# Kernel tuning notes

Hardware: AMD Instinct MI355X
Metric: run time of the kernel (lower is better)

Reference implementation:

```python
import jax, jax.numpy as jnp
from jax import lax
import numpy as np

H = 32  # hidden size
D = 1   # input size


def setup_inputs() -> dict:
    key = jax.random.key(0)
    ks = jax.random.split(key, 7)
    B, T = 4096, 1024
    s_ih = 1.0 / np.sqrt(H)
    return {
        "x": jax.random.normal(ks[0], (B, T, D), dtype=jnp.float32),
        # PyTorch LSTM params, gate order i,f,g,o stacked along dim 0
        "W_ih": jax.random.uniform(ks[1], (4 * H, D), jnp.float32, -s_ih, s_ih),
        "W_hh": jax.random.uniform(ks[2], (4 * H, H), jnp.float32, -s_ih, s_ih),
        "b_ih": jax.random.uniform(ks[3], (4 * H,), jnp.float32, -s_ih, s_ih),
        "b_hh": jax.random.uniform(ks[4], (4 * H,), jnp.float32, -s_ih, s_ih),
        "fc_W": jax.random.uniform(ks[5], (1, H), jnp.float32, -s_ih, s_ih),
        "fc_b": jax.random.uniform(ks[6], (1,), jnp.float32, -s_ih, s_ih),
    }


def reference(x, W_ih, W_hh, b_ih, b_hh, fc_W, fc_b):
    B = x.shape[0]
    # Precompute input contribution for all timesteps: [B, T, 4H]
    x_proj = jnp.einsum("btd,gd->btg", x, W_ih) + b_ih + b_hh
    h0 = jnp.zeros((B, H), dtype=x.dtype)
    c0 = jnp.zeros((B, H), dtype=x.dtype)

    def step(carry, xg):
        h, c = carry
        gates = xg + h @ W_hh.T  # [B, 4H]
        i, f, g, o = jnp.split(gates, 4, axis=-1)
        i = jax.nn.sigmoid(i)
        f = jax.nn.sigmoid(f)
        g = jnp.tanh(g)
        o = jax.nn.sigmoid(o)
        c = f * c + i * g
        h = o * jnp.tanh(c)
        return (h, c), None

    (h_last, _), _ = lax.scan(step, (h0, c0), jnp.swapaxes(x_proj, 0, 1))
    return h_last @ fc_W.T + fc_b  # [B, 1]
```

## Files before the change

kernel.cpp:

```cpp
#include <hip/hip_runtime.h>
#include <math.h>


#define HH 32
#define TT 1024
#define BPB 4
#define NT 128

typedef _Float16 half8 __attribute__((ext_vector_type(8)));
typedef float    f32x4 __attribute__((ext_vector_type(4)));

__global__ __attribute__((amdgpu_flat_work_group_size(NT, NT),
                          amdgpu_waves_per_eu(2, 2)))
void lstm_vp(const float* __restrict__ x,
             const float* __restrict__ W_ih,
             const float* __restrict__ W_hh,
             const float* __restrict__ b_ih,
             const float* __restrict__ b_hh,
             const float* __restrict__ fc_W,
             const float* __restrict__ fc_b,
             float* __restrict__ out)
{
    __shared__ _Float16 xw[BPB * TT];
    __shared__ __align__(16) _Float16 hx[2][BPB][HH];
    __shared__ float fo[BPB];

    const int tid  = threadIdx.x;
    const int P    = tid >> 6;
    const int lane = tid & 63;
    const int q    = lane >> 4;
    const int n    = lane & 15;
    const int u    = 2 * n + P;
    const int gb0  = blockIdx.x * BPB;

    {
        const float4* xg = (const float4*)(x + (size_t)gb0 * TT);
        #pragma unroll
        for (int it = 0; it < (BPB * TT / 4) / NT; ++it) {
            const int idx = it * NT + tid;
            const float4 v = xg[idx];
            _Float16* dst = &xw[idx * 4];
            dst[0] = (_Float16)v.x; dst[1] = (_Float16)v.y;
            dst[2] = (_Float16)v.z; dst[3] = (_Float16)v.w;
        }
    }

    const float L1 = 1.4426950408889634f;

    half8 wf[4];
    #pragma unroll
    for (int g = 0; g < 4; ++g) {
        const float s = (g == 2) ? -2.0f * L1 : -L1;
        const float* arow = W_hh + (size_t)(32 * g + 2 * n + P) * HH + 8 * q;
        #pragma unroll
        for (int j = 0; j < 8; ++j)
            wf[g][j] = (_Float16)(arow[j] * s);
    }

    float wx[4], bb[4];
    #pragma unroll
    for (int g = 0; g < 4; ++g) {
        const float s = (g == 2) ? -2.0f * L1 : -L1;
        wx[g] = W_ih[g * HH + u] * s;
        bb[g] = (b_ih[g * HH + u] + b_hh[g * HH + u]) * s;
    }

    hx[0][q][u] = (_Float16)0.0f;
    __syncthreads();

    const half8* hr0 = (const half8*)&hx[0][n >> 2][8 * q];
    const half8* hr1 = (const half8*)&hx[1][n >> 2][8 * q];

    float c = 0.0f, h = 0.0f;

    const half8* xp = (const half8*)&xw[q * TT];
    half8 xcur = xp[0];

    #pragma unroll 1
    for (int tc = 0; tc < TT / 8; ++tc) {
        const half8 xv8 = xcur;
        xcur = xp[(tc + 1) & (TT / 8 - 1)];

        float xf[8];
        #pragma unroll
        for (int j = 0; j < 8; ++j) xf[j] = (float)xv8[j];

        #pragma unroll
        for (int tt = 0; tt < 8; ++tt) {
            const half8 av = (tt & 1) ? *hr1 : *hr0;

            const float xv = xf[tt];
            float qq[4];
            #pragma unroll
            for (int g = 0; g < 4; ++g)
                qq[g] = fmaf(xv, wx[g], bb[g]);

            const f32x4 zero = {0.0f, 0.0f, 0.0f, 0.0f};
            f32x4 acc[4];
            #pragma unroll
            for (int g = 0; g < 4; ++g) {
                acc[g] = __builtin_amdgcn_mfma_f32_16x16x32_f16(
                             av, wf[g], zero, 0, 0, 0);
                asm("" : "+v"(acc[g]));
            }

            const float ea = __builtin_amdgcn_exp2f(acc[0][0] + qq[0]);
            const float eb = __builtin_amdgcn_exp2f(acc[1][0] + qq[1]);
            const float ed = __builtin_amdgcn_exp2f(acc[2][0] + qq[2]);
            const float ee = __builtin_amdgcn_exp2f(acc[3][0] + qq[3]);

            const float uu = 1.0f + ea, vv = 1.0f + ed, ww = 1.0f + eb;
            const float uv  = uu * vv;
            const float num = fmaf(c, uv, ww * (2.0f - vv));
            c = num * __builtin_amdgcn_rcpf(uv * ww);

            const float marg = fminf(c * (-2.0f * L1), 126.0f);
            const float m = __builtin_amdgcn_exp2f(marg);
            h = (1.0f - m) * __builtin_amdgcn_rcpf((1.0f + ee) * (1.0f + m));

            hx[(tt & 1) ^ 1][q][u] = (_Float16)h;
            __syncthreads();
        }
    }

    float pr = h * fc_W[u];
    pr += __shfl_xor(pr, 1, 64);
    pr += __shfl_xor(pr, 2, 64);
    pr += __shfl_xor(pr, 4, 64);
    pr += __shfl_xor(pr, 8, 64);
    if (P == 1 && n == 0) fo[q] = pr;
    __syncthreads();
    if (P == 0 && n == 0)
        out[gb0 + q] = pr + fo[q] + fc_b[0];
}

extern "C" void kernel_launch(void* const* d_in, const int* in_sizes, int n_in,
                              void* d_out, int out_size, void* d_ws, size_t ws_size,
                              hipStream_t stream) {
    const float* x    = (const float*)d_in[0];
    const float* W_ih = (const float*)d_in[1];
    const float* W_hh = (const float*)d_in[2];
    const float* b_ih = (const float*)d_in[3];
    const float* b_hh = (const float*)d_in[4];
    const float* fc_W = (const float*)d_in[5];
    const float* fc_b = (const float*)d_in[6];
    float* out = (float*)d_out;

    const int B = in_sizes[0] / TT;
    dim3 grid(B / BPB), block(NT);
    lstm_vp<<<grid, block, 0, stream>>>(x, W_ih, W_hh, b_ih, b_hh,
                                        fc_W, fc_b, out);
}
```

Baseline: 315.1 us.

## Process two interleaved batch groups per block to hide recurrence latency

Doubles the batch rows per block from 4 to 8, with each thread carrying two independent LSTM chains (A and B). The two chains' MFMAs and transcendental ops interleave, filling latency stalls in the serial recurrence and halving the number of blocks and barriers per batch element. In exchange, register and LDS use per block rise and the grid has half as many blocks, which may reduce occupancy.

```diff
diff --git a/kernel.cpp b/kernel.cpp
--- a/kernel.cpp
+++ b/kernel.cpp
@@ -4,14 +4,14 @@
 
 #define HH 32
 #define TT 1024
-#define BPB 4
+#define BPB 8
 #define NT 128
 
 typedef _Float16 half8 __attribute__((ext_vector_type(8)));
 typedef float    f32x4 __attribute__((ext_vector_type(4)));
 
 __global__ __attribute__((amdgpu_flat_work_group_size(NT, NT),
-                          amdgpu_waves_per_eu(2, 2)))
+                          amdgpu_waves_per_eu(1, 2)))
 void lstm_vp(const float* __restrict__ x,
              const float* __restrict__ W_ih,
              const float* __restrict__ W_hh,
@@ -65,73 +65,106 @@
         bb[g] = (b_ih[g * HH + u] + b_hh[g * HH + u]) * s;
     }
 
-    hx[0][q][u] = (_Float16)0.0f;
+    hx[0][q][u]     = (_Float16)0.0f;
+    hx[0][4 + q][u] = (_Float16)0.0f;
     __syncthreads();
 
-    const half8* hr0 = (const half8*)&hx[0][n >> 2][8 * q];
-    const half8* hr1 = (const half8*)&hx[1][n >> 2][8 * q];
+    const half8* hrA0 = (const half8*)&hx[0][n >> 2][8 * q];
+    const half8* hrA1 = (const half8*)&hx[1][n >> 2][8 * q];
+    const half8* hrB0 = (const half8*)&hx[0][4 + (n >> 2)][8 * q];
+    const half8* hrB1 = (const half8*)&hx[1][4 + (n >> 2)][8 * q];
 
-    float c = 0.0f, h = 0.0f;
+    float cA = 0.0f, hA = 0.0f, cB = 0.0f, hB = 0.0f;
 
-    const half8* xp = (const half8*)&xw[q * TT];
-    half8 xcur = xp[0];
+    const half8* xpA = (const half8*)&xw[q * TT];
+    const half8* xpB = (const half8*)&xw[(4 + q) * TT];
+    half8 xcurA = xpA[0];
+    half8 xcurB = xpB[0];
 
     #pragma unroll 1
     for (int tc = 0; tc < TT / 8; ++tc) {
-        const half8 xv8 = xcur;
-        xcur = xp[(tc + 1) & (TT / 8 - 1)];
+        const half8 xvA = xcurA;
+        const half8 xvB = xcurB;
+        const int nc = (tc + 1) & (TT / 8 - 1);
+        xcurA = xpA[nc];
+        xcurB = xpB[nc];
 
-        float xf[8];
+        float xfA[8], xfB[8];
         #pragma unroll
-        for (int j = 0; j < 8; ++j) xf[j] = (float)xv8[j];
+        for (int j = 0; j < 8; ++j) { xfA[j] = (float)xvA[j]; xfB[j] = (float)xvB[j]; }
 
         #pragma unroll
         for (int tt = 0; tt < 8; ++tt) {
-            const half8 av = (tt & 1) ? *hr1 : *hr0;
+            const half8 avA = (tt & 1) ? *hrA1 : *hrA0;
+            const half8 avB = (tt & 1) ? *hrB1 : *hrB0;
 
-            const float xv = xf[tt];
-            float qq[4];
+            float qqA[4], qqB[4];
             #pragma unroll
-            for (int g = 0; g < 4; ++g)
-                qq[g] = fmaf(xv, wx[g], bb[g]);
+            for (int g = 0; g < 4; ++g) {
+                qqA[g] = fmaf(xfA[tt], wx[g], bb[g]);
+                qqB[g] = fmaf(xfB[tt], wx[g], bb[g]);
+            }
 
             const f32x4 zero = {0.0f, 0.0f, 0.0f, 0.0f};
-            f32x4 acc[4];
+            f32x4 accA[4], accB[4];
             #pragma unroll
             for (int g = 0; g < 4; ++g) {
-                acc[g] = __builtin_amdgcn_mfma_f32_16x16x32_f16(
-                             av, wf[g], zero, 0, 0, 0);
-                asm("" : "+v"(acc[g]));
+                accA[g] = __builtin_amdgcn_mfma_f32_16x16x32_f16(
+                              avA, wf[g], zero, 0, 0, 0);
+                asm("" : "+v"(accA[g]));
+            }
+            #pragma unroll
+            for (int g = 0; g < 4; ++g) {
+                accB[g] = __builtin_amdgcn_mfma_f32_16x16x32_f16(
+                              avB, wf[g], zero, 0, 0, 0);
+                asm("" : "+v"(accB[g]));
             }
 
-            const float ea = __builtin_amdgcn_exp2f(acc[0][0] + qq[0]);
-            const float eb = __builtin_amdgcn_exp2f(acc[1][0] + qq[1]);
-            const float ed = __builtin_amdgcn_exp2f(acc[2][0] + qq[2]);
-            const float ee = __builtin_amdgcn_exp2f(acc[3][0] + qq[3]);
+            const float eaA = __builtin_amdgcn_exp2f(accA[0][0] + qqA[0]);
+            const float eaB = __builtin_amdgcn_exp2f(accB[0][0] + qqB[0]);
+            const float ebA = __builtin_amdgcn_exp2f(accA[1][0] + qqA[1]);
+            const float ebB = __builtin_amdgcn_exp2f(accB[1][0] + qqB[1]);
+            const float edA = __builtin_amdgcn_exp2f(accA[2][0] + qqA[2]);
+            const float edB = __builtin_amdgcn_exp2f(accB[2][0] + qqB[2]);
+            const float eeA = __builtin_amdgcn_exp2f(accA[3][0] + qqA[3]);
+            const float eeB = __builtin_amdgcn_exp2f(accB[3][0] + qqB[3]);
 
-            const float uu = 1.0f + ea, vv = 1.0f + ed, ww = 1.0f + eb;
-            const float uv  = uu * vv;
-            const float num = fmaf(c, uv, ww * (2.0f - vv));
-            c = num * __builtin_amdgcn_rcpf(uv * ww);
+            const float uuA = 1.0f + eaA, vvA = 1.0f + edA, wwA = 1.0f + ebA;
+            const float uuB = 1.0f + eaB, vvB = 1.0f + edB, wwB = 1.0f + ebB;
+            const float uvA = uuA * vvA;
+            const float uvB = uuB * vvB;
+            const float numA = fmaf(cA, uvA, wwA * (2.0f - vvA));
+            const float numB = fmaf(cB, uvB, wwB * (2.0f - vvB));
+            cA = numA * __builtin_amdgcn_rcpf(uvA * wwA);
+            cB = numB * __builtin_amdgcn_rcpf(uvB * wwB);
 
-            const float marg = fminf(c * (-2.0f * L1), 126.0f);
-            const float m = __builtin_amdgcn_exp2f(marg);
-            h = (1.0f - m) * __builtin_amdgcn_rcpf((1.0f + ee) * (1.0f + m));
+            const float mgA = fminf(cA * (-2.0f * L1), 126.0f);
+            const float mgB = fminf(cB * (-2.0f * L1), 126.0f);
+            const float mA = __builtin_amdgcn_exp2f(mgA);
+            const float mB = __builtin_amdgcn_exp2f(mgB);
+            hA = (1.0f - mA) * __builtin_amdgcn_rcpf((1.0f + eeA) * (1.0f + mA));
+            hB = (1.0f - mB) * __builtin_amdgcn_rcpf((1.0f + eeB) * (1.0f + mB));
 
-            hx[(tt & 1) ^ 1][q][u] = (_Float16)h;
+            const int ns = (tt & 1) ^ 1;
+            hx[ns][q][u]     = (_Float16)hA;
+            hx[ns][4 + q][u] = (_Float16)hB;
             __syncthreads();
         }
     }
 
-    float pr = h * fc_W[u];
-    pr += __shfl_xor(pr, 1, 64);
-    pr += __shfl_xor(pr, 2, 64);
-    pr += __shfl_xor(pr, 4, 64);
-    pr += __shfl_xor(pr, 8, 64);
-    if (P == 1 && n == 0) fo[q] = pr;
+    float prA = hA * fc_W[u];
+    float prB = hB * fc_W[u];
+    #pragma unroll
+    for (int d = 1; d <= 8; d <<= 1) {
+        prA += __shfl_xor(prA, d, 64);
+        prB += __shfl_xor(prB, d, 64);
+    }
+    if (P == 1 && n == 0) { fo[q] = prA; fo[4 + q] = prB; }
     __syncthreads();
-    if (P == 0 && n == 0)
-        out[gb0 + q] = pr + fo[q] + fc_b[0];
+    if (P == 0 && n == 0) {
+        out[gb0 + q]     = prA + fo[q]     + fc_b[0];
+        out[gb0 + 4 + q] = prB + fo[4 + q] + fc_b[0];
+    }
 }
 
 extern "C" void kernel_launch(void* const* d_in, const int* in_sizes, int n_in,
```

Result: slower. 562.4 us (+78.5%).
